# Optimization experiments

Measured on AMD Instinct MI355X. Metric: run time of the kernel, lower is better.

## Reference

```python
import jax, jax.numpy as jnp
import numpy as np

N_NODES = 100000
IN_DIM = 64
HIDDEN = 128
N_EDGES = 1000000


def _linear_params(key, fan_in, fan_out):
    # torch nn.Linear default init: U(-1/sqrt(fan_in), 1/sqrt(fan_in))
    kW, kb = jax.random.split(key)
    bound = 1.0 / np.sqrt(fan_in)
    W = jax.random.uniform(kW, (fan_in, fan_out), jnp.float32, -bound, bound)
    b = jax.random.uniform(kb, (fan_out,), jnp.float32, -bound, bound)
    return W, b


def setup_inputs() -> dict:
    key = jax.random.key(0)
    kx, ke, k1, k2, k3, k4 = jax.random.split(key, 6)
    x = jax.random.normal(kx, (N_NODES, IN_DIM), jnp.float32)
    edge_index = jax.random.randint(ke, (2, N_EDGES), 0, N_NODES, jnp.int64)
    W1, b1 = _linear_params(k1, IN_DIM * 2, HIDDEN)
    W2, b2 = _linear_params(k2, HIDDEN, HIDDEN)
    W3, b3 = _linear_params(k3, HIDDEN, HIDDEN)
    W4, b4 = _linear_params(k4, HIDDEN, 1)
    return {"x": x, "edge_index": edge_index,
            "W1": W1, "b1": b1, "W2": W2, "b2": b2,
            "W3": W3, "b3": b3, "W4": W4, "b4": b4}


def reference(x, edge_index, W1, b1, W2, b2, W3, b3, W4, b4):
    src, dst = edge_index[0], edge_index[1]
    # [E, 2*in_dim] gathered edge inputs
    edge_inputs = jnp.concatenate([x[src], x[dst]], axis=1)
    h = jnp.tanh(edge_inputs @ W1 + b1)
    h = jnp.tanh(h @ W2 + b2)
    h = jnp.tanh(h @ W3 + b3)
    out = jax.nn.sigmoid(h @ W4 + b4)
    return out.squeeze(-1)  # [E]
```

## Files before the change

### kernel.cpp

```cpp
#include <hip/hip_runtime.h>
#include <cstdint>

typedef _Float16 f16x8 __attribute__((ext_vector_type(8)));
typedef float    f32x4 __attribute__((ext_vector_type(4)));

#define E_TOTAL   1000000
#define N_NODES   100000
#define NROUNDS   3907
#define GRID_MAIN 512
#define SCL       2.8853900817779268f

__device__ __forceinline__ float tanh_pre(float a) {
  float e = __builtin_amdgcn_exp2f(a);
  return 1.0f - 2.0f * __builtin_amdgcn_rcpf(1.0f + e);
}
__device__ __forceinline__ float fast_sigmoid(float x) {
  float e = __builtin_amdgcn_exp2f(x * -1.4426950408889634f);
  return __builtin_amdgcn_rcpf(1.0f + e);
}
__device__ __forceinline__ uint32_t pack2(float a, float b) {
  return __builtin_bit_cast(uint32_t, __builtin_amdgcn_cvt_pkrtz(a, b));
}
__device__ __forceinline__ f16x8 asfrag(const uint32_t (&u)[4]) {
  uint4 v;
  v.x = u[0]; v.y = u[1]; v.z = u[2]; v.w = u[3];
  return __builtin_bit_cast(f16x8, v);
}

__global__ void kconv_x(const float* __restrict__ x, _Float16* __restrict__ xh) {
  int i = blockIdx.x * 256 + threadIdx.x;
  if (i >= (N_NODES * 64) / 8) return;
  const float4* p = (const float4*)x + (size_t)i * 2;
  float4 a = p[0], b = p[1];
  f16x8 o = {(_Float16)a.x, (_Float16)a.y, (_Float16)a.z, (_Float16)a.w,
             (_Float16)b.x, (_Float16)b.y, (_Float16)b.z, (_Float16)b.w};
  *((f16x8*)xh + i) = o;
}

__global__ void kswz_w(const float* __restrict__ W1, const float* __restrict__ W2,
                       const float* __restrict__ W3, _Float16* __restrict__ wswz) {
  int idx = blockIdx.x * 256 + threadIdx.x;
  if (idx >= 49152) return;
  int jj = idx & 7;
  int l  = (idx >> 3) & 63;
  int s  = (idx >> 9) & 3;
  int T  = (idx >> 11) & 7;
  int L  = idx >> 14;
  int k  = 32 * s + 4 * (l >> 4) + (jj & 3) + 16 * (jj >> 2);
  int n  = 16 * T + (l & 15);
  const float* W = (L == 0) ? W1 : ((L == 1) ? W2 : W3);
  wswz[idx] = (_Float16)(W[k * 128 + n] * SCL);
}

template <int L>
__device__ __forceinline__ void mlp_layer(const _Float16* lds_w, const float* lds_b,
                                          int lane,
                                          const uint32_t (&Bin)[2][4][4],
                                          uint32_t (&Bout)[2][4][4]) {
  const int g = lane >> 4;
#pragma unroll
  for (int T = 0; T < 8; ++T) {
    const f32x4 bf = *(const f32x4*)(lds_b + L * 128 + T * 16 + g * 4);
    f32x4 acc0 = bf, acc1 = bf;
#pragma unroll
    for (int s = 0; s < 4; ++s) {
      const f16x8 W = *(const f16x8*)(lds_w + (size_t)(((L * 8 + T) * 4 + s) * 512) + lane * 8);
      acc0 = __builtin_amdgcn_mfma_f32_16x16x32_f16(W, asfrag(Bin[0][s]), acc0, 0, 0, 0);
      acc1 = __builtin_amdgcn_mfma_f32_16x16x32_f16(W, asfrag(Bin[1][s]), acc1, 0, 0, 0);
    }
    const int si = T >> 1, d = (T & 1) * 2;
    Bout[0][si][d]     = pack2(tanh_pre(acc0[0]), tanh_pre(acc0[1]));
    Bout[0][si][d + 1] = pack2(tanh_pre(acc0[2]), tanh_pre(acc0[3]));
    Bout[1][si][d]     = pack2(tanh_pre(acc1[0]), tanh_pre(acc1[1]));
    Bout[1][si][d + 1] = pack2(tanh_pre(acc1[2]), tanh_pre(acc1[3]));
  }
}

__device__ __forceinline__ void mlp_out(const _Float16* __restrict__ gw3,
                                        const float* lds_b, int lane,
                                        const uint32_t (&Bin)[2][4][4],
                                        float (&dot)[2]) {
  const int g = lane >> 4;
  dot[0] = dot[1] = 0.f;
#pragma unroll
  for (int T = 0; T < 8; ++T) {
    const f32x4 bf = *(const f32x4*)(lds_b + 256 + T * 16 + g * 4);
    const f32x4 wf = *(const f32x4*)(lds_b + 384 + T * 16 + g * 4);
    f32x4 acc0 = bf, acc1 = bf;
#pragma unroll
    for (int s = 0; s < 4; ++s) {
      const f16x8 W = *(const f16x8*)(gw3 + (size_t)((T * 4 + s) * 512) + lane * 8);
      acc0 = __builtin_amdgcn_mfma_f32_16x16x32_f16(W, asfrag(Bin[0][s]), acc0, 0, 0, 0);
      acc1 = __builtin_amdgcn_mfma_f32_16x16x32_f16(W, asfrag(Bin[1][s]), acc1, 0, 0, 0);
    }
    dot[0] += tanh_pre(acc0[0]) * wf[0] + tanh_pre(acc0[1]) * wf[1]
            + tanh_pre(acc0[2]) * wf[2] + tanh_pre(acc0[3]) * wf[3];
    dot[1] += tanh_pre(acc1[0]) * wf[0] + tanh_pre(acc1[1]) * wf[1]
            + tanh_pre(acc1[2]) * wf[2] + tanh_pre(acc1[3]) * wf[3];
  }
}

template <bool XH>
__global__ __launch_bounds__(512)
__attribute__((amdgpu_num_vgpr(128)))
void edge_mlp(
    const int* __restrict__ eidx,
    const _Float16* __restrict__ xh,
    const float* __restrict__ xf,
    const _Float16* __restrict__ wswz,
    const float* __restrict__ b1, const float* __restrict__ b2,
    const float* __restrict__ b3, const float* __restrict__ w4,
    const float* __restrict__ b4g,
    float* __restrict__ out) {
  extern __shared__ char smem[];
  _Float16* lds_w = (_Float16*)smem;
  float*    lds_b = (float*)(smem + 65536);
  const _Float16* gw3 = wswz + 32768;

  const int tid = threadIdx.x;
  {
    const uint4* src = (const uint4*)wswz;
    uint4* dst = (uint4*)smem;
#pragma unroll
    for (int i = 0; i < 8; ++i) dst[tid + i * 512] = src[tid + i * 512];
  }
  if (tid < 128) {
    lds_b[tid]       = b1[tid] * SCL;
    lds_b[128 + tid] = b2[tid] * SCL;
    lds_b[256 + tid] = b3[tid] * SCL;
    lds_b[384 + tid] = w4[tid];
  }
  __syncthreads();

  const float b4v = b4g[0];
  const int wid = tid >> 6, lane = tid & 63;
  const int c = lane & 15, g = lane >> 4;

  int pre_s[2], pre_d[2];
#pragma unroll
  for (int t = 0; t < 2; ++t) {
    int e  = blockIdx.x * 256 + wid * 32 + t * 16 + c;
    int ee = (e < E_TOTAL) ? e : 0;
    pre_s[t] = eidx[ee];
    pre_d[t] = eidx[E_TOTAL + ee];
  }

  for (int round = blockIdx.x; round < NROUNDS; round += GRID_MAIN) {
    const int ebase = round * 256 + wid * 32;

    uint32_t B0[2][4][4];
#pragma unroll
    for (int t = 0; t < 2; ++t) {
      int sN = pre_s[t];
      int dN = pre_d[t];
      if (XH) {
        const _Float16* ps = xh + (size_t)sN * 64 + g * 4;
        const _Float16* pd = xh + (size_t)dN * 64 + g * 4;
#pragma unroll
        for (int sp = 0; sp < 2; ++sp) {
#pragma unroll
          for (int h = 0; h < 2; ++h) {
            uint2 rs = *(const uint2*)(ps + sp * 32 + h * 16);
            uint2 rd = *(const uint2*)(pd + sp * 32 + h * 16);
            B0[t][sp][h * 2]         = rs.x;
            B0[t][sp][h * 2 + 1]     = rs.y;
            B0[t][2 + sp][h * 2]     = rd.x;
            B0[t][2 + sp][h * 2 + 1] = rd.y;
          }
        }
      } else {
        const float* ps = xf + (size_t)sN * 64 + g * 4;
        const float* pd = xf + (size_t)dN * 64 + g * 4;
#pragma unroll
        for (int sp = 0; sp < 2; ++sp) {
#pragma unroll
          for (int h = 0; h < 2; ++h) {
            float4 fs = *(const float4*)(ps + sp * 32 + h * 16);
            float4 fd = *(const float4*)(pd + sp * 32 + h * 16);
            B0[t][sp][h * 2]         = pack2(fs.x, fs.y);
            B0[t][sp][h * 2 + 1]     = pack2(fs.z, fs.w);
            B0[t][2 + sp][h * 2]     = pack2(fd.x, fd.y);
            B0[t][2 + sp][h * 2 + 1] = pack2(fd.z, fd.w);
          }
        }
      }
    }

    {
      int nr = round + GRID_MAIN;
      if (nr < NROUNDS) {
#pragma unroll
        for (int t = 0; t < 2; ++t) {
          int e  = nr * 256 + wid * 32 + t * 16 + c;
          int ee = (e < E_TOTAL) ? e : 0;
          pre_s[t] = eidx[ee];
          pre_d[t] = eidx[E_TOTAL + ee];
        }
      }
    }

    uint32_t B1r[2][4][4], B2r[2][4][4];
    mlp_layer<0>(lds_w, lds_b, lane, B0, B1r);
    mlp_layer<1>(lds_w, lds_b, lane, B1r, B2r);

    float dot[2];
    mlp_out(gw3, lds_b, lane, B2r, dot);

#pragma unroll
    for (int t = 0; t < 2; ++t) {
      float v = dot[t];
      v += __shfl_xor(v, 16);
      v += __shfl_xor(v, 32);
      dot[t] = v;
    }
    if (g == 0) {
#pragma unroll
      for (int t = 0; t < 2; ++t) {
        int e = ebase + t * 16 + c;
        if (e < E_TOTAL) out[e] = fast_sigmoid(dot[t] + b4v);
      }
    }
    __builtin_amdgcn_sched_barrier(0);
  }
}

extern "C" void kernel_launch(void* const* d_in, const int* in_sizes, int n_in,
                              void* d_out, int out_size, void* d_ws, size_t ws_size,
                              hipStream_t stream) {
  (void)in_sizes; (void)n_in; (void)out_size;
  const float* x  = (const float*)d_in[0];
  const int* eidx = (const int*)d_in[1];
  const float* W1 = (const float*)d_in[2];
  const float* b1 = (const float*)d_in[3];
  const float* W2 = (const float*)d_in[4];
  const float* b2 = (const float*)d_in[5];
  const float* W3 = (const float*)d_in[6];
  const float* b3 = (const float*)d_in[7];
  const float* w4 = (const float*)d_in[8];
  const float* b4 = (const float*)d_in[9];
  float* out = (float*)d_out;

  const size_t XH_BYTES   = (size_t)N_NODES * 64 * 2;
  const size_t WS_W_BYTES = 49152 * 2;
  const bool xh_ok = ws_size >= XH_BYTES + WS_W_BYTES;

  _Float16* ws_xh = (_Float16*)d_ws;
  _Float16* ws_w  = (_Float16*)((char*)d_ws + (xh_ok ? XH_BYTES : 0));

  kswz_w<<<192, 256, 0, stream>>>(W1, W2, W3, ws_w);
  if (xh_ok) kconv_x<<<3125, 256, 0, stream>>>(x, ws_xh);

  const size_t lds_bytes = 65536 + 2048;
  if (xh_ok) {
    edge_mlp<true><<<GRID_MAIN, 512, lds_bytes, stream>>>(
        eidx, ws_xh, x, ws_w, b1, b2, b3, w4, b4, out);
  } else {
    edge_mlp<false><<<GRID_MAIN, 512, lds_bytes, stream>>>(
        eidx, ws_xh, x, ws_w, b1, b2, b3, w4, b4, out);
  }
}
```

Before: 151.2 us.

## Prefetch next round's node features into LDS via async global_load_lds

Node feature rows for the next round are now fetched directly into per-wave LDS buffers with asynchronous global-to-LDS loads, issued after the second MLP layer so they overlap the third layer's compute. The first layer's input fragments are then read from LDS after a vmcnt wait, not gathered from global memory at the start of each round. Bias scaling moves to a small prep kernel, and the layer-3 bias and output weights are read from global memory, freeing LDS. LDS use grows to about 130KB per block, which limits occupancy to one block per CU, and the vmcnt(0) wait also stalls on any other outstanding global loads.

Measured after the change: 212.4 us. 1.41x slower.

```diff
diff --git a/kernel.cpp b/kernel.cpp
--- a/kernel.cpp
+++ b/kernel.cpp
@@ -25,6 +25,11 @@
   uint4 v;
   v.x = u[0]; v.y = u[1]; v.z = u[2]; v.w = u[3];
   return __builtin_bit_cast(f16x8, v);
+}
+__device__ __forceinline__ void gload_lds16(const void* g, void* l) {
+  __builtin_amdgcn_global_load_lds(
+      (const __attribute__((address_space(1))) void*)g,
+      (__attribute__((address_space(3))) void*)(uintptr_t)l, 16, 0, 0);
 }
 
 __global__ void kconv_x(const float* __restrict__ x, _Float16* __restrict__ xh) {
@@ -52,6 +57,19 @@
   wswz[idx] = (_Float16)(W[k * 128 + n] * SCL);
 }
 
+__global__ void kprep_b(const float* __restrict__ b1, const float* __restrict__ b2,
+                        const float* __restrict__ b3, const float* __restrict__ w4,
+                        float* __restrict__ bscl) {
+  int i = blockIdx.x * 256 + threadIdx.x;
+  if (i >= 512) return;
+  int r = i & 127;
+  float v = (i < 128) ? b1[r] * SCL
+          : (i < 256) ? b2[r] * SCL
+          : (i < 384) ? b3[r] * SCL
+          :             w4[r];
+  bscl[i] = v;
+}
+
 template <int L>
 __device__ __forceinline__ void mlp_layer(const _Float16* lds_w, const float* lds_b,
                                           int lane,
@@ -77,15 +95,15 @@
 }
 
 __device__ __forceinline__ void mlp_out(const _Float16* __restrict__ gw3,
-                                        const float* lds_b, int lane,
+                                        const float* __restrict__ gb, int lane,
                                         const uint32_t (&Bin)[2][4][4],
                                         float (&dot)[2]) {
   const int g = lane >> 4;
   dot[0] = dot[1] = 0.f;
 #pragma unroll
   for (int T = 0; T < 8; ++T) {
-    const f32x4 bf = *(const f32x4*)(lds_b + 256 + T * 16 + g * 4);
-    const f32x4 wf = *(const f32x4*)(lds_b + 384 + T * 16 + g * 4);
+    const f32x4 bf = *(const f32x4*)(gb + T * 16 + g * 4);
+    const f32x4 wf = *(const f32x4*)(gb + 128 + T * 16 + g * 4);
     f32x4 acc0 = bf, acc1 = bf;
 #pragma unroll
     for (int s = 0; s < 4; ++s) {
@@ -99,6 +117,10 @@
             + tanh_pre(acc1[2]) * wf[2] + tanh_pre(acc1[3]) * wf[3];
   }
 }
+
+#define LDS_B_OFF   65536
+#define LDS_G_OFF   66560
+#define LDS_TOTAL   (66560 + 8 * 8192)
 
 template <bool XH>
 __global__ __launch_bounds__(512)
@@ -108,14 +130,13 @@
     const _Float16* __restrict__ xh,
     const float* __restrict__ xf,
     const _Float16* __restrict__ wswz,
-    const float* __restrict__ b1, const float* __restrict__ b2,
-    const float* __restrict__ b3, const float* __restrict__ w4,
-    const float* __restrict__ b4g,
+    const float* __restrict__ bscl,
     float* __restrict__ out) {
   extern __shared__ char smem[];
   _Float16* lds_w = (_Float16*)smem;
-  float*    lds_b = (float*)(smem + 65536);
+  float*    lds_b = (float*)(smem + LDS_B_OFF);
   const _Float16* gw3 = wswz + 32768;
+  const float*    gb  = bscl + 256;
 
   const int tid = threadIdx.x;
   {
@@ -124,17 +145,13 @@
 #pragma unroll
     for (int i = 0; i < 8; ++i) dst[tid + i * 512] = src[tid + i * 512];
   }
-  if (tid < 128) {
-    lds_b[tid]       = b1[tid] * SCL;
-    lds_b[128 + tid] = b2[tid] * SCL;
-    lds_b[256 + tid] = b3[tid] * SCL;
-    lds_b[384 + tid] = w4[tid];
-  }
+  if (tid < 256) lds_b[tid] = bscl[tid];
   __syncthreads();
 
-  const float b4v = b4g[0];
+  const float b4v = gb[256];
   const int wid = tid >> 6, lane = tid & 63;
   const int c = lane & 15, g = lane >> 4;
+  char* gbuf = smem + LDS_G_OFF + wid * 8192;
 
   int pre_s[2], pre_d[2];
 #pragma unroll
@@ -144,31 +161,46 @@
     pre_s[t] = eidx[ee];
     pre_d[t] = eidx[E_TOTAL + ee];
   }
+  if (XH) {
+#pragma unroll
+    for (int t = 0; t < 2; ++t) {
+      const _Float16* ns = xh + (size_t)pre_s[t] * 64 + g * 8;
+      const _Float16* nd = xh + (size_t)pre_d[t] * 64 + g * 8;
+      char* cb = gbuf + t * 4096;
+      gload_lds16(ns,      cb);
+      gload_lds16(ns + 32, cb + 1024);
+      gload_lds16(nd,      cb + 2048);
+      gload_lds16(nd + 32, cb + 3072);
+    }
+  }
 
   for (int round = blockIdx.x; round < NROUNDS; round += GRID_MAIN) {
     const int ebase = round * 256 + wid * 32;
 
     uint32_t B0[2][4][4];
-#pragma unroll
-    for (int t = 0; t < 2; ++t) {
-      int sN = pre_s[t];
-      int dN = pre_d[t];
-      if (XH) {
-        const _Float16* ps = xh + (size_t)sN * 64 + g * 4;
-        const _Float16* pd = xh + (size_t)dN * 64 + g * 4;
-#pragma unroll
-        for (int sp = 0; sp < 2; ++sp) {
-#pragma unroll
-          for (int h = 0; h < 2; ++h) {
-            uint2 rs = *(const uint2*)(ps + sp * 32 + h * 16);
-            uint2 rd = *(const uint2*)(pd + sp * 32 + h * 16);
-            B0[t][sp][h * 2]         = rs.x;
-            B0[t][sp][h * 2 + 1]     = rs.y;
-            B0[t][2 + sp][h * 2]     = rd.x;
-            B0[t][2 + sp][h * 2 + 1] = rd.y;
+    if (XH) {
+      asm volatile("s_waitcnt vmcnt(0)" ::: "memory");
+      __builtin_amdgcn_sched_barrier(0);
+#pragma unroll
+      for (int t = 0; t < 2; ++t) {
+        const char* cb = gbuf + t * 4096 + c * 16 + (g >> 1) * 256 + (g & 1) * 8;
+#pragma unroll
+        for (int n = 0; n < 2; ++n) {
+#pragma unroll
+          for (int sp = 0; sp < 2; ++sp) {
+            const char* p = cb + (n * 2 + sp) * 1024;
+            uint2 lo = *(const uint2*)(p);
+            uint2 hi = *(const uint2*)(p + 512);
+            B0[t][n * 2 + sp][0] = lo.x; B0[t][n * 2 + sp][1] = lo.y;
+            B0[t][n * 2 + sp][2] = hi.x; B0[t][n * 2 + sp][3] = hi.y;
           }
         }
-      } else {
+      }
+    } else {
+#pragma unroll
+      for (int t = 0; t < 2; ++t) {
+        int sN = pre_s[t];
+        int dN = pre_d[t];
         const float* ps = xf + (size_t)sN * 64 + g * 4;
         const float* pd = xf + (size_t)dN * 64 + g * 4;
 #pragma unroll
@@ -188,14 +220,13 @@
 
     {
       int nr = round + GRID_MAIN;
-      if (nr < NROUNDS) {
-#pragma unroll
-        for (int t = 0; t < 2; ++t) {
-          int e  = nr * 256 + wid * 32 + t * 16 + c;
-          int ee = (e < E_TOTAL) ? e : 0;
-          pre_s[t] = eidx[ee];
-          pre_d[t] = eidx[E_TOTAL + ee];
-        }
+      int base = (nr < NROUNDS) ? nr * 256 + wid * 32 : 0;
+#pragma unroll
+      for (int t = 0; t < 2; ++t) {
+        int e  = base + t * 16 + c;
+        int ee = (e < E_TOTAL) ? e : 0;
+        pre_s[t] = eidx[ee];
+        pre_d[t] = eidx[E_TOTAL + ee];
       }
     }
 
@@ -203,8 +234,21 @@
     mlp_layer<0>(lds_w, lds_b, lane, B0, B1r);
     mlp_layer<1>(lds_w, lds_b, lane, B1r, B2r);
 
+    if (XH) {
+#pragma unroll
+      for (int t = 0; t < 2; ++t) {
+        const _Float16* ns = xh + (size_t)pre_s[t] * 64 + g * 8;
+        const _Float16* nd = xh + (size_t)pre_d[t] * 64 + g * 8;
+        char* cb = gbuf + t * 4096;
+        gload_lds16(ns,      cb);
+        gload_lds16(ns + 32, cb + 1024);
+        gload_lds16(nd,      cb + 2048);
+        gload_lds16(nd + 32, cb + 3072);
+      }
+    }
+
     float dot[2];
-    mlp_out(gw3, lds_b, lane, B2r, dot);
+    mlp_out(gw3, gb, lane, B2r, dot);
 
 #pragma unroll
     for (int t = 0; t < 2; ++t) {
@@ -242,20 +286,23 @@
 
   const size_t XH_BYTES   = (size_t)N_NODES * 64 * 2;
   const size_t WS_W_BYTES = 49152 * 2;
-  const bool xh_ok = ws_size >= XH_BYTES + WS_W_BYTES;
+  const size_t WS_B_BYTES = (512 + 4) * 4;
+  const bool xh_ok = ws_size >= XH_BYTES + WS_W_BYTES + WS_B_BYTES;
 
   _Float16* ws_xh = (_Float16*)d_ws;
   _Float16* ws_w  = (_Float16*)((char*)d_ws + (xh_ok ? XH_BYTES : 0));
+  float*    bscl  = (float*)((char*)ws_w + WS_W_BYTES);
 
   kswz_w<<<192, 256, 0, stream>>>(W1, W2, W3, ws_w);
+  kprep_b<<<2, 256, 0, stream>>>(b1, b2, b3, w4, bscl);
+  hipMemcpyAsync(bscl + 512, b4, 4, hipMemcpyDeviceToDevice, stream);
   if (xh_ok) kconv_x<<<3125, 256, 0, stream>>>(x, ws_xh);
 
-  const size_t lds_bytes = 65536 + 2048;
   if (xh_ok) {
-    edge_mlp<true><<<GRID_MAIN, 512, lds_bytes, stream>>>(
-        eidx, ws_xh, x, ws_w, b1, b2, b3, w4, b4, out);
+    edge_mlp<true><<<GRID_MAIN, 512, LDS_TOTAL, stream>>>(
+        eidx, ws_xh, x, ws_w, bscl, out);
   } else {
-    edge_mlp<false><<<GRID_MAIN, 512, lds_bytes, stream>>>(
-        eidx, ws_xh, x, ws_w, b1, b2, b3, w4, b4, out);
-  }
-}
+    edge_mlp<false><<<GRID_MAIN, 512, LDS_TOTAL, stream>>>(
+        eidx, ws_xh, x, ws_w, bscl, out);
+  }
+}
```
